# Kernel optimization log

Hardware: AMD Instinct MI355X
Metric: run time of the kernel (lower is better)

## Reference

```python
import jax, jax.numpy as jnp
import numpy as np

NEG_SLOPE = 0.2  # LeakyReLU slope used by standard GAT


def setup_inputs() -> dict:
    key = jax.random.key(0)
    k1, k2, k3, k4, k5, k6 = jax.random.split(key, 6)
    N, E, F_in, F_out = 100000, 1600000, 256, 128
    x = jax.random.normal(k1, (N, F_in), dtype=jnp.float32)
    edge_index = jax.random.randint(k2, (2, E), 0, N, dtype=jnp.int32)
    W = jax.random.normal(k3, (F_in, F_out), dtype=jnp.float32) * (1.0 / np.sqrt(F_in))
    a_src = jax.random.normal(k4, (F_out,), dtype=jnp.float32) * 0.1
    a_dst = jax.random.normal(k5, (F_out,), dtype=jnp.float32) * 0.1
    return {"x": x, "edge_index": edge_index, "W": W, "a_src": a_src, "a_dst": a_dst}


def reference(x, edge_index, W, a_src, a_dst):
    N = x.shape[0]
    src, dst = edge_index[0], edge_index[1]

    Wh = x @ W                               # [N, F_out]
    alpha_src = Wh @ a_src                   # [N]
    alpha_dst = Wh @ a_dst                   # [N]

    e = alpha_src[src] + alpha_dst[dst]      # [E] raw edge scores
    e = jnp.where(e > 0, e, NEG_SLOPE * e)   # LeakyReLU(0.2)

    # segment softmax over incoming edges of each destination node
    seg_max = jax.ops.segment_max(e, dst, num_segments=N)          # [N]
    seg_max = jnp.where(jnp.isfinite(seg_max), seg_max, 0.0)
    e_exp = jnp.exp(e - seg_max[dst])                               # [E]
    denom = jax.ops.segment_sum(e_exp, dst, num_segments=N)         # [N]
    alpha = e_exp / (denom[dst] + 1e-16)                            # [E]

    # weighted aggregation of source messages
    msgs = alpha[:, None] * Wh[src]                                  # [E, F_out]
    out = jax.ops.segment_sum(msgs, dst, num_segments=N)             # [N, F_out]
    return jax.nn.elu(out)
```

## Files before the change

kernel.cpp:

```cpp
#include <hip/hip_runtime.h>
#include <math.h>

#define NEG_SLOPE 0.2f
#define BINSH 8
#define BCAP 6144

typedef __attribute__((ext_vector_type(8))) short bf16x8;
typedef __attribute__((ext_vector_type(4))) float f32x4;

__device__ inline unsigned short f2b(float f) {
  union { float f; unsigned u; } v; v.f = f;
  unsigned r = v.u + 0x7fffu + ((v.u >> 16) & 1u);
  return (unsigned short)(r >> 16);
}

__launch_bounds__(256)
__global__ void k_work1(const float* __restrict__ W, unsigned short* __restrict__ WtB,
                        const int* __restrict__ src, const int* __restrict__ dst,
                        int* __restrict__ cursor, unsigned* __restrict__ binned,
                        int E, int NBUK) {
  int bid = blockIdx.x;
  int t = threadIdx.x;
  if (bid < 128) {
    int i = bid * 256 + t;
    int k = i >> 7, n = i & 127;
    WtB[n * 256 + k] = f2b(W[(size_t)k * 128 + n]);
    return;
  }
  __shared__ int lh[512];
  for (int c = t; c < NBUK; c += 256) lh[c] = 0;
  __syncthreads();
  int base = (bid - 128) * 2048;
  int bq[8], rq[8]; unsigned pq[8];
#pragma unroll
  for (int q = 0; q < 8; ++q) {
    int j = base + q * 256 + t;
    if (j < E) {
      int d = dst[j], s = src[j];
      bq[q] = d >> BINSH;
      pq[q] = ((unsigned)s << 8) | (unsigned)(d & 255);
      rq[q] = atomicAdd(&lh[bq[q]], 1);
    } else bq[q] = -1;
  }
  __syncthreads();
  for (int c = t; c < NBUK; c += 256) { int cnt = lh[c]; if (cnt) lh[c] = atomicAdd(&cursor[c], cnt); }
  __syncthreads();
#pragma unroll
  for (int q = 0; q < 8; ++q)
    if (bq[q] >= 0) binned[(size_t)bq[q] * BCAP + lh[bq[q]] + rq[q]] = pq[q];
}

__launch_bounds__(256, 4)
__global__ void k_work2(const float* __restrict__ x, const unsigned short* __restrict__ WtB,
                        const float* __restrict__ a_src, const float* __restrict__ a_dst,
                        unsigned short* __restrict__ WhB, float* __restrict__ asrc,
                        float* __restrict__ adst, int N, int nGemm,
                        const unsigned* __restrict__ binned, const int* __restrict__ cursor,
                        int* __restrict__ offsets, int* __restrict__ degs,
                        int* __restrict__ csr) {
  int t = threadIdx.x;
  if ((int)blockIdx.x < nGemm) {
    __shared__ unsigned short Cs[128 * 136];
    int lane = t & 63, wid = t >> 6;
    int lr = lane & 15, lh2 = lane >> 4;
    int m0 = blockIdx.x * 128;
    int row0 = m0 + wid * 32 + lr;
    int row1 = row0 + 16;
    int r0c = row0 < N ? row0 : N - 1;
    int r1c = row1 < N ? row1 : N - 1;
    const float* xp0 = x + (size_t)r0c * 256 + lh2 * 8;
    const float* xp1 = x + (size_t)r1c * 256 + lh2 * 8;

    f32x4 acc[2][8];
#pragma unroll
    for (int rf = 0; rf < 2; ++rf)
#pragma unroll
      for (int f = 0; f < 8; ++f) acc[rf][f] = (f32x4){0.f, 0.f, 0.f, 0.f};

#pragma unroll
    for (int ks = 0; ks < 8; ++ks) {
      float4 u0 = *(const float4*)(xp0 + ks * 32);
      float4 u1 = *(const float4*)(xp0 + ks * 32 + 4);
      float4 v0 = *(const float4*)(xp1 + ks * 32);
      float4 v1 = *(const float4*)(xp1 + ks * 32 + 4);
      bf16x8 a0, a1;
      a0[0] = (short)f2b(u0.x); a0[1] = (short)f2b(u0.y);
      a0[2] = (short)f2b(u0.z); a0[3] = (short)f2b(u0.w);
      a0[4] = (short)f2b(u1.x); a0[5] = (short)f2b(u1.y);
      a0[6] = (short)f2b(u1.z); a0[7] = (short)f2b(u1.w);
      a1[0] = (short)f2b(v0.x); a1[1] = (short)f2b(v0.y);
      a1[2] = (short)f2b(v0.z); a1[3] = (short)f2b(v0.w);
      a1[4] = (short)f2b(v1.x); a1[5] = (short)f2b(v1.y);
      a1[6] = (short)f2b(v1.z); a1[7] = (short)f2b(v1.w);
#pragma unroll
      for (int f = 0; f < 8; ++f) {
        bf16x8 b = *(const bf16x8*)(WtB + ((lr + 16 * f) * 256 + ks * 32 + lh2 * 8));
        acc[0][f] = __builtin_amdgcn_mfma_f32_16x16x32_bf16(a0, b, acc[0][f], 0, 0, 0);
        acc[1][f] = __builtin_amdgcn_mfma_f32_16x16x32_bf16(a1, b, acc[1][f], 0, 0, 0);
      }
    }

    float asv[8], adv[8];
#pragma unroll
    for (int f = 0; f < 8; ++f) { asv[f] = a_src[lr + 16 * f]; adv[f] = a_dst[lr + 16 * f]; }
    float as_p[2][4] = {}, ad_p[2][4] = {};
#pragma unroll
    for (int rf = 0; rf < 2; ++rf)
#pragma unroll
      for (int f = 0; f < 8; ++f)
#pragma unroll
        for (int r = 0; r < 4; ++r) {
          as_p[rf][r] += acc[rf][f][r] * asv[f];
          ad_p[rf][r] += acc[rf][f][r] * adv[f];
        }
#pragma unroll
    for (int off = 1; off < 16; off <<= 1)
#pragma unroll
      for (int rf = 0; rf < 2; ++rf)
#pragma unroll
        for (int r = 0; r < 4; ++r) {
          as_p[rf][r] += __shfl_xor(as_p[rf][r], off);
          ad_p[rf][r] += __shfl_xor(ad_p[rf][r], off);
        }
    if (lr == 0) {
#pragma unroll
      for (int rf = 0; rf < 2; ++rf)
#pragma unroll
        for (int r = 0; r < 4; ++r) {
          int m = m0 + wid * 32 + rf * 16 + lh2 * 4 + r;
          if (m < N) { asrc[m] = as_p[rf][r]; adst[m] = ad_p[rf][r]; }
        }
    }

#pragma unroll
    for (int rf = 0; rf < 2; ++rf)
#pragma unroll
      for (int f = 0; f < 8; ++f)
#pragma unroll
        for (int r = 0; r < 4; ++r)
          Cs[(wid * 32 + rf * 16 + lh2 * 4 + r) * 136 + lr + 16 * f] = f2b(acc[rf][f][r]);
    __syncthreads();
#pragma unroll
    for (int i = 0; i < 8; ++i) {
      int chunk = i * 256 + t;
      int row = chunk >> 4, c8 = chunk & 15;
      int m = m0 + row;
      if (m < N) {
        bf16x8 v = *(const bf16x8*)(Cs + row * 136 + c8 * 8);
        *(bf16x8*)(WhB + (size_t)m * 128 + c8 * 8) = v;
      }
    }
    return;
  }

  {
    int b = blockIdx.x - nGemm;
    int lane = t & 63, wid = t >> 6;
    int beg = b * BCAP, end = beg + cursor[b];
    int node0 = b << BINSH;
    int nn = N - node0; if (nn > 256) nn = 256; if (nn < 0) nn = 0;
    __shared__ int ldeg[256];
    __shared__ int lcur[256];
    __shared__ int wp[4];
    ldeg[t] = 0;
    __syncthreads();
    for (int j = beg + t; j < end; j += 256) atomicAdd(&ldeg[binned[j] & 255u], 1);
    __syncthreads();
    int v = (t < nn) ? ldeg[t] : 0;
    int incl = v;
#pragma unroll
    for (int off = 1; off < 64; off <<= 1) { int u = __shfl_up(incl, off); if (lane >= off) incl += u; }
    if (lane == 63) wp[wid] = incl;
    __syncthreads();
    int add = 0;
    for (int k = 0; k < wid; ++k) add += wp[k];
    int ex = add + incl - v;
    if (t < nn) { offsets[node0 + t] = beg + ex; degs[node0 + t] = v; lcur[t] = ex; }
    __syncthreads();
    for (int j = beg + t; j < end; j += 256) {
      unsigned e = binned[j];
      int r = atomicAdd(&lcur[e & 255u], 1);
      csr[beg + r] = (int)(e >> 8);
    }
  }
}

__launch_bounds__(256)
__global__ void k_agg(const int* __restrict__ csr, const int* __restrict__ offsets,
                      const int* __restrict__ degs,
                      const unsigned short* __restrict__ WhB, const float* __restrict__ asrc,
                      const float* __restrict__ adst, float* __restrict__ out, int N) {
  int gt = blockIdx.x * blockDim.x + threadIdx.x;
  int wave = gt >> 6;
  int lane = gt & 63;
  int lq = lane & 15;
  int g = lane >> 4;
  int node = wave * 4 + g;
  if (node >= N) return;
  int beg = offsets[node];
  int end = beg + degs[node];
  float ad = adst[node];
  float acc[8] = {};
  float psum = 0.f;
  for (int chunk = beg; chunk < end; chunk += 16) {
    int j = chunk + lq;
    float p = 0.f; int mys = 0;
    if (j < end) {
      mys = csr[j];
      float e = asrc[mys] + ad;
      e = e > 0.f ? e : NEG_SLOPE * e;
      p = __expf(e);
    }
    psum += p;
#pragma unroll
    for (int tt = 0; tt < 8; ++tt) {
      float pt = __shfl(p, tt, 16);
      int st = __shfl(mys, tt, 16);
      uint4 v = *(const uint4*)(WhB + (size_t)(unsigned)st * 128u + lq * 8);
      acc[0] = fmaf(pt, __uint_as_float(v.x << 16), acc[0]);
      acc[1] = fmaf(pt, __uint_as_float(v.x & 0xffff0000u), acc[1]);
      acc[2] = fmaf(pt, __uint_as_float(v.y << 16), acc[2]);
      acc[3] = fmaf(pt, __uint_as_float(v.y & 0xffff0000u), acc[3]);
      acc[4] = fmaf(pt, __uint_as_float(v.z << 16), acc[4]);
      acc[5] = fmaf(pt, __uint_as_float(v.z & 0xffff0000u), acc[5]);
      acc[6] = fmaf(pt, __uint_as_float(v.w << 16), acc[6]);
      acc[7] = fmaf(pt, __uint_as_float(v.w & 0xffff0000u), acc[7]);
    }
    __builtin_amdgcn_sched_barrier(0);
#pragma unroll
    for (int tt = 8; tt < 16; ++tt) {
      float pt = __shfl(p, tt, 16);
      int st = __shfl(mys, tt, 16);
      uint4 v = *(const uint4*)(WhB + (size_t)(unsigned)st * 128u + lq * 8);
      acc[0] = fmaf(pt, __uint_as_float(v.x << 16), acc[0]);
      acc[1] = fmaf(pt, __uint_as_float(v.x & 0xffff0000u), acc[1]);
      acc[2] = fmaf(pt, __uint_as_float(v.y << 16), acc[2]);
      acc[3] = fmaf(pt, __uint_as_float(v.y & 0xffff0000u), acc[3]);
      acc[4] = fmaf(pt, __uint_as_float(v.z << 16), acc[4]);
      acc[5] = fmaf(pt, __uint_as_float(v.z & 0xffff0000u), acc[5]);
      acc[6] = fmaf(pt, __uint_as_float(v.w << 16), acc[6]);
      acc[7] = fmaf(pt, __uint_as_float(v.w & 0xffff0000u), acc[7]);
    }
  }
  psum += __shfl_xor(psum, 1);
  psum += __shfl_xor(psum, 2);
  psum += __shfl_xor(psum, 4);
  psum += __shfl_xor(psum, 8);
  float inv = 1.f / (psum + 1e-16f);
  size_t obase = (size_t)node * 128 + lq * 8;
  float r[8];
#pragma unroll
  for (int i = 0; i < 8; ++i) {
    float o = acc[i] * inv;
    r[i] = o > 0.f ? o : __expf(o) - 1.f;
  }
  f32x4 lo = {r[0], r[1], r[2], r[3]};
  f32x4 hi = {r[4], r[5], r[6], r[7]};
  __builtin_nontemporal_store(lo, (f32x4*)(out + obase));
  __builtin_nontemporal_store(hi, (f32x4*)(out + obase + 4));
}

extern "C" void kernel_launch(void* const* d_in, const int* in_sizes, int n_in,
                              void* d_out, int out_size, void* d_ws, size_t ws_size,
                              hipStream_t stream) {
  const float* x = (const float*)d_in[0];
  const int* ei = (const int*)d_in[1];
  const float* W = (const float*)d_in[2];
  const float* a_src = (const float*)d_in[3];
  const float* a_dst = (const float*)d_in[4];
  int N = in_sizes[0] / 256;
  int E = in_sizes[1] / 2;
  const int* src = ei;
  const int* dst = ei + E;
  float* out = (float*)d_out;
  int NBUK = (N + 255) >> BINSH;
  size_t REG = (size_t)NBUK * BCAP;

  unsigned short* WhB = (unsigned short*)d_ws;
  unsigned* binned = (unsigned*)(WhB + (size_t)N * 128);
  int* csr = (int*)(binned + REG);
  float* asrc = (float*)(csr + REG);
  float* adst = asrc + N;
  unsigned short* WtB = (unsigned short*)(adst + N);
  int* cursor = (int*)(WtB + 32768);
  int* offsets = cursor + NBUK;
  int* degs = offsets + N;

  int nBinA = (E + 2047) / 2048;
  int nGemm = (N + 127) / 128;

  hipMemsetAsync(cursor, 0, (size_t)NBUK * sizeof(int), stream);
  k_work1<<<128 + nBinA, 256, 0, stream>>>(W, WtB, src, dst, cursor, binned, E, NBUK);
  k_work2<<<nGemm + NBUK, 256, 0, stream>>>(x, WtB, a_src, a_dst, WhB, asrc, adst, N, nGemm,
                                            binned, cursor, offsets, degs, csr);
  k_agg<<<(N + 15) / 16, 256, 0, stream>>>(csr, offsets, degs, WhB, asrc, adst, out, N);
}
```

Baseline: 157.3 us.

## Stage x tile in swizzled LDS as bf16 and halve GEMM block rows

After: 171.5 us. +9.0%, slower.

```diff
diff --git a/kernel.cpp b/kernel.cpp
--- a/kernel.cpp
+++ b/kernel.cpp
@@ -7,6 +7,7 @@
 
 typedef __attribute__((ext_vector_type(8))) short bf16x8;
 typedef __attribute__((ext_vector_type(4))) float f32x4;
+typedef __attribute__((ext_vector_type(8))) unsigned short us8;
 
 __device__ inline unsigned short f2b(float f) {
   union { float f; unsigned u; } v; v.f = f;
@@ -60,95 +61,90 @@
                         int* __restrict__ csr) {
   int t = threadIdx.x;
   if ((int)blockIdx.x < nGemm) {
-    __shared__ unsigned short Cs[128 * 136];
+    __shared__ __align__(16) unsigned short As[64 * 256];
     int lane = t & 63, wid = t >> 6;
     int lr = lane & 15, lh2 = lane >> 4;
-    int m0 = blockIdx.x * 128;
-    int row0 = m0 + wid * 32 + lr;
-    int row1 = row0 + 16;
-    int r0c = row0 < N ? row0 : N - 1;
-    int r1c = row1 < N ? row1 : N - 1;
-    const float* xp0 = x + (size_t)r0c * 256 + lh2 * 8;
-    const float* xp1 = x + (size_t)r1c * 256 + lh2 * 8;
-
-    f32x4 acc[2][8];
-#pragma unroll
-    for (int rf = 0; rf < 2; ++rf)
-#pragma unroll
-      for (int f = 0; f < 8; ++f) acc[rf][f] = (f32x4){0.f, 0.f, 0.f, 0.f};
-
+    int m0 = blockIdx.x * 64;
+
+    float4 ubuf[16];
+#pragma unroll
+    for (int i = 0; i < 8; ++i) {
+      int f8 = i * 256 + t;
+      int row = f8 >> 5, c8 = f8 & 31;
+      int m = m0 + row; if (m >= N) m = N - 1;
+      const float* xp = x + (size_t)m * 256 + c8 * 8;
+      ubuf[2 * i] = *(const float4*)(xp);
+      ubuf[2 * i + 1] = *(const float4*)(xp + 4);
+    }
+#pragma unroll
+    for (int i = 0; i < 8; ++i) {
+      int f8 = i * 256 + t;
+      int row = f8 >> 5, c8 = f8 & 31;
+      float4 u0 = ubuf[2 * i], u1 = ubuf[2 * i + 1];
+      us8 o;
+      o[0] = f2b(u0.x); o[1] = f2b(u0.y); o[2] = f2b(u0.z); o[3] = f2b(u0.w);
+      o[4] = f2b(u1.x); o[5] = f2b(u1.y); o[6] = f2b(u1.z); o[7] = f2b(u1.w);
+      *(us8*)(As + row * 256 + ((c8 ^ (row & 15)) << 3)) = o;
+    }
+    __syncthreads();
+
+    f32x4 acc[8];
+#pragma unroll
+    for (int f = 0; f < 8; ++f) acc[f] = (f32x4){0.f, 0.f, 0.f, 0.f};
+    int rowr = wid * 16 + lr;
+    int rswz = rowr & 15;
+    const unsigned short* Arow = As + rowr * 256;
 #pragma unroll
     for (int ks = 0; ks < 8; ++ks) {
-      float4 u0 = *(const float4*)(xp0 + ks * 32);
-      float4 u1 = *(const float4*)(xp0 + ks * 32 + 4);
-      float4 v0 = *(const float4*)(xp1 + ks * 32);
-      float4 v1 = *(const float4*)(xp1 + ks * 32 + 4);
-      bf16x8 a0, a1;
-      a0[0] = (short)f2b(u0.x); a0[1] = (short)f2b(u0.y);
-      a0[2] = (short)f2b(u0.z); a0[3] = (short)f2b(u0.w);
-      a0[4] = (short)f2b(u1.x); a0[5] = (short)f2b(u1.y);
-      a0[6] = (short)f2b(u1.z); a0[7] = (short)f2b(u1.w);
-      a1[0] = (short)f2b(v0.x); a1[1] = (short)f2b(v0.y);
-      a1[2] = (short)f2b(v0.z); a1[3] = (short)f2b(v0.w);
-      a1[4] = (short)f2b(v1.x); a1[5] = (short)f2b(v1.y);
-      a1[6] = (short)f2b(v1.z); a1[7] = (short)f2b(v1.w);
+      bf16x8 a = *(const bf16x8*)(Arow + (((ks * 4 + lh2) ^ rswz) << 3));
 #pragma unroll
       for (int f = 0; f < 8; ++f) {
         bf16x8 b = *(const bf16x8*)(WtB + ((lr + 16 * f) * 256 + ks * 32 + lh2 * 8));
-        acc[0][f] = __builtin_amdgcn_mfma_f32_16x16x32_bf16(a0, b, acc[0][f], 0, 0, 0);
-        acc[1][f] = __builtin_amdgcn_mfma_f32_16x16x32_bf16(a1, b, acc[1][f], 0, 0, 0);
+        acc[f] = __builtin_amdgcn_mfma_f32_16x16x32_bf16(a, b, acc[f], 0, 0, 0);
       }
     }
 
     float asv[8], adv[8];
 #pragma unroll
     for (int f = 0; f < 8; ++f) { asv[f] = a_src[lr + 16 * f]; adv[f] = a_dst[lr + 16 * f]; }
-    float as_p[2][4] = {}, ad_p[2][4] = {};
-#pragma unroll
-    for (int rf = 0; rf < 2; ++rf)
-#pragma unroll
-      for (int f = 0; f < 8; ++f)
-#pragma unroll
-        for (int r = 0; r < 4; ++r) {
-          as_p[rf][r] += acc[rf][f][r] * asv[f];
-          ad_p[rf][r] += acc[rf][f][r] * adv[f];
-        }
+    float as_p[4] = {}, ad_p[4] = {};
+#pragma unroll
+    for (int f = 0; f < 8; ++f)
+#pragma unroll
+      for (int r = 0; r < 4; ++r) {
+        as_p[r] += acc[f][r] * asv[f];
+        ad_p[r] += acc[f][r] * adv[f];
+      }
 #pragma unroll
     for (int off = 1; off < 16; off <<= 1)
 #pragma unroll
-      for (int rf = 0; rf < 2; ++rf)
-#pragma unroll
-        for (int r = 0; r < 4; ++r) {
-          as_p[rf][r] += __shfl_xor(as_p[rf][r], off);
-          ad_p[rf][r] += __shfl_xor(ad_p[rf][r], off);
-        }
+      for (int r = 0; r < 4; ++r) {
+        as_p[r] += __shfl_xor(as_p[r], off);
+        ad_p[r] += __shfl_xor(ad_p[r], off);
+      }
     if (lr == 0) {
 #pragma unroll
-      for (int rf = 0; rf < 2; ++rf)
-#pragma unroll
-        for (int r = 0; r < 4; ++r) {
-          int m = m0 + wid * 32 + rf * 16 + lh2 * 4 + r;
-          if (m < N) { asrc[m] = as_p[rf][r]; adst[m] = ad_p[rf][r]; }
-        }
-    }
-
-#pragma unroll
-    for (int rf = 0; rf < 2; ++rf)
-#pragma unroll
-      for (int f = 0; f < 8; ++f)
-#pragma unroll
-        for (int r = 0; r < 4; ++r)
-          Cs[(wid * 32 + rf * 16 + lh2 * 4 + r) * 136 + lr + 16 * f] = f2b(acc[rf][f][r]);
-    __syncthreads();
-#pragma unroll
-    for (int i = 0; i < 8; ++i) {
+      for (int r = 0; r < 4; ++r) {
+        int m = m0 + wid * 16 + lh2 * 4 + r;
+        if (m < N) { asrc[m] = as_p[r]; adst[m] = ad_p[r]; }
+      }
+    }
+
+    __syncthreads();
+    unsigned short* Cs = As;
+#pragma unroll
+    for (int f = 0; f < 8; ++f)
+#pragma unroll
+      for (int r = 0; r < 4; ++r)
+        Cs[(wid * 16 + lh2 * 4 + r) * 136 + lr + 16 * f] = f2b(acc[f][r]);
+    __syncthreads();
+#pragma unroll
+    for (int i = 0; i < 4; ++i) {
       int chunk = i * 256 + t;
-      int row = chunk >> 4, c8 = chunk & 15;
+      int row = chunk >> 4, c8o = chunk & 15;
       int m = m0 + row;
-      if (m < N) {
-        bf16x8 v = *(const bf16x8*)(Cs + row * 136 + c8 * 8);
-        *(bf16x8*)(WhB + (size_t)m * 128 + c8 * 8) = v;
-      }
+      if (m < N)
+        *(us8*)(WhB + (size_t)m * 128 + c8o * 8) = *(const us8*)(Cs + row * 136 + c8o * 8);
     }
     return;
   }
@@ -287,7 +283,7 @@
   int* degs = offsets + N;
 
   int nBinA = (E + 2047) / 2048;
-  int nGemm = (N + 127) / 128;
+  int nGemm = (N + 63) / 64;
 
   hipMemsetAsync(cursor, 0, (size_t)NBUK * sizeof(int), stream);
   k_work1<<<128 + nBinA, 256, 0, stream>>>(W, WtB, src, dst, cursor, binned, E, NBUK);
```

## Stage x tiles into LDS via direct global-to-LDS loads with XOR swizzle

Applied to the files above, without the earlier changes.

After: 159.2 us. About the same (+1.2%).

```diff
diff --git a/kernel.cpp b/kernel.cpp
--- a/kernel.cpp
+++ b/kernel.cpp
@@ -7,11 +7,29 @@
 
 typedef __attribute__((ext_vector_type(8))) short bf16x8;
 typedef __attribute__((ext_vector_type(4))) float f32x4;
+typedef __attribute__((ext_vector_type(8))) unsigned short us8;
 
 __device__ inline unsigned short f2b(float f) {
   union { float f; unsigned u; } v; v.f = f;
   unsigned r = v.u + 0x7fffu + ((v.u >> 16) & 1u);
   return (unsigned short)(r >> 16);
+}
+
+__device__ inline bf16x8 cvt8(f32x4 a, f32x4 b) {
+  unsigned r0, r1, r2, r3;
+  asm("v_cvt_pk_bf16_f32 %0, %1, %2" : "=v"(r0) : "v"(a[0]), "v"(a[1]));
+  asm("v_cvt_pk_bf16_f32 %0, %1, %2" : "=v"(r1) : "v"(a[2]), "v"(a[3]));
+  asm("v_cvt_pk_bf16_f32 %0, %1, %2" : "=v"(r2) : "v"(b[0]), "v"(b[1]));
+  asm("v_cvt_pk_bf16_f32 %0, %1, %2" : "=v"(r3) : "v"(b[2]), "v"(b[3]));
+  union { unsigned u[4]; bf16x8 v; } o;
+  o.u[0] = r0; o.u[1] = r1; o.u[2] = r2; o.u[3] = r3;
+  return o.v;
+}
+
+__device__ inline void gload_lds16(const float* g, void* l) {
+  __builtin_amdgcn_global_load_lds(
+      (const __attribute__((address_space(1))) void*)g,
+      (__attribute__((address_space(3))) void*)l, 16, 0, 0);
 }
 
 __launch_bounds__(256)
@@ -60,16 +78,12 @@
                         int* __restrict__ csr) {
   int t = threadIdx.x;
   if ((int)blockIdx.x < nGemm) {
-    __shared__ unsigned short Cs[128 * 136];
+    __shared__ __align__(16) unsigned char sbuf[34816];
+    float* As = (float*)sbuf;
+    unsigned short* Cs = (unsigned short*)sbuf;
     int lane = t & 63, wid = t >> 6;
     int lr = lane & 15, lh2 = lane >> 4;
     int m0 = blockIdx.x * 128;
-    int row0 = m0 + wid * 32 + lr;
-    int row1 = row0 + 16;
-    int r0c = row0 < N ? row0 : N - 1;
-    int r1c = row1 < N ? row1 : N - 1;
-    const float* xp0 = x + (size_t)r0c * 256 + lh2 * 8;
-    const float* xp1 = x + (size_t)r1c * 256 + lh2 * 8;
 
     f32x4 acc[2][8];
 #pragma unroll
@@ -77,27 +91,46 @@
 #pragma unroll
       for (int f = 0; f < 8; ++f) acc[rf][f] = (f32x4){0.f, 0.f, 0.f, 0.f};
 
-#pragma unroll
-    for (int ks = 0; ks < 8; ++ks) {
-      float4 u0 = *(const float4*)(xp0 + ks * 32);
-      float4 u1 = *(const float4*)(xp0 + ks * 32 + 4);
-      float4 v0 = *(const float4*)(xp1 + ks * 32);
-      float4 v1 = *(const float4*)(xp1 + ks * 32 + 4);
-      bf16x8 a0, a1;
-      a0[0] = (short)f2b(u0.x); a0[1] = (short)f2b(u0.y);
-      a0[2] = (short)f2b(u0.z); a0[3] = (short)f2b(u0.w);
-      a0[4] = (short)f2b(u1.x); a0[5] = (short)f2b(u1.y);
-      a0[6] = (short)f2b(u1.z); a0[7] = (short)f2b(u1.w);
-      a1[0] = (short)f2b(v0.x); a1[1] = (short)f2b(v0.y);
-      a1[2] = (short)f2b(v0.z); a1[3] = (short)f2b(v0.w);
-      a1[4] = (short)f2b(v1.x); a1[5] = (short)f2b(v1.y);
-      a1[6] = (short)f2b(v1.z); a1[7] = (short)f2b(v1.w);
-#pragma unroll
-      for (int f = 0; f < 8; ++f) {
-        bf16x8 b = *(const bf16x8*)(WtB + ((lr + 16 * f) * 256 + ks * 32 + lh2 * 8));
-        acc[0][f] = __builtin_amdgcn_mfma_f32_16x16x32_bf16(a0, b, acc[0][f], 0, 0, 0);
-        acc[1][f] = __builtin_amdgcn_mfma_f32_16x16x32_bf16(a1, b, acc[1][f], 0, 0, 0);
+    int r0 = wid * 32 + lr;
+    int r1 = r0 + 16;
+    const float* A0 = As + r0 * 64;
+    const float* A1 = As + r1 * 64;
+    int srow = lane >> 4;
+    int scol = lane & 15;
+
+    for (int s = 0; s < 4; ++s) {
+      int k0 = s * 64;
+#pragma unroll
+      for (int i = 0; i < 8; ++i) {
+        int bc = i * 256 + wid * 64;
+        int row = (bc >> 4) + srow;
+        int m = m0 + row; if (m >= N) m = N - 1;
+        int cs = scol ^ (row & 15);
+        gload_lds16(x + (size_t)m * 256 + k0 + cs * 4, (char*)As + bc * 16);
       }
+      bf16x8 bb[8];
+#pragma unroll
+      for (int f = 0; f < 8; ++f)
+        bb[f] = *(const bf16x8*)(WtB + (lr + 16 * f) * 256 + k0 + lh2 * 8);
+      __syncthreads();
+#pragma unroll
+      for (int ks2 = 0; ks2 < 2; ++ks2) {
+        int j0 = ks2 * 8 + lh2 * 2;
+        f32x4 u0 = *(const f32x4*)(A0 + (((j0) ^ lr) << 2));
+        f32x4 u1 = *(const f32x4*)(A0 + (((j0 + 1) ^ lr) << 2));
+        f32x4 v0 = *(const f32x4*)(A1 + (((j0) ^ lr) << 2));
+        f32x4 v1 = *(const f32x4*)(A1 + (((j0 + 1) ^ lr) << 2));
+        bf16x8 a0 = cvt8(u0, u1);
+        bf16x8 a1 = cvt8(v0, v1);
+#pragma unroll
+        for (int f = 0; f < 8; ++f) {
+          bf16x8 b = ks2 ? *(const bf16x8*)(WtB + (lr + 16 * f) * 256 + k0 + 32 + lh2 * 8)
+                         : bb[f];
+          acc[0][f] = __builtin_amdgcn_mfma_f32_16x16x32_bf16(a0, b, acc[0][f], 0, 0, 0);
+          acc[1][f] = __builtin_amdgcn_mfma_f32_16x16x32_bf16(a1, b, acc[1][f], 0, 0, 0);
+        }
+      }
+      __syncthreads();
     }
 
     float asv[8], adv[8];
@@ -145,10 +178,8 @@
       int chunk = i * 256 + t;
       int row = chunk >> 4, c8 = chunk & 15;
       int m = m0 + row;
-      if (m < N) {
-        bf16x8 v = *(const bf16x8*)(Cs + row * 136 + c8 * 8);
-        *(bf16x8*)(WhB + (size_t)m * 128 + c8 * 8) = v;
-      }
+      if (m < N)
+        *(us8*)(WhB + (size_t)m * 128 + c8 * 8) = *(const us8*)(Cs + row * 136 + c8 * 8);
     }
     return;
   }
```
